# Performance work log

Measured on AMD Instinct MI355X. Metric: run time of the kernel, lower is better.

The kernel has to match this reference:

```python
import jax, jax.numpy as jnp
import numpy as np

B, H, W = 8, 128, 128
WIDTH, MODES = 32, 12
NL = 6


def _spectral_conv(x, w):
    # x: [B,C,H,W] real; w: [2, Cin, Cout, m, m, 2] (real/imag packed)
    b, c, h, ww = x.shape
    m = w.shape[3]
    xf = jnp.fft.rfft2(x)  # [B,C,H,W//2+1] complex
    w1 = w[0, ..., 0] + 1j * w[0, ..., 1]
    w2 = w[1, ..., 0] + 1j * w[1, ..., 1]
    top = jnp.einsum('bixy,ioxy->boxy', xf[:, :, :m, :m], w1)
    bot = jnp.einsum('bixy,ioxy->boxy', xf[:, :, -m:, :m], w2)
    out = jnp.zeros((b, w.shape[2], h, ww // 2 + 1), dtype=xf.dtype)
    out = out.at[:, :, :m, :m].set(top).at[:, :, -m:, :m].set(bot)
    return jnp.fft.irfft2(out, s=(h, ww))


def _conv1x1(x, wgt, bia):
    # x: [B,C,H,W], wgt: [O,C], bia: [O]
    return jnp.einsum('bchw,oc->bohw', x, wgt) + bia[None, :, None, None]


def _gelu(x):
    return jax.nn.gelu(x, approximate=False)


def setup_inputs() -> dict:
    key = jax.random.key(0)
    ks = jax.random.split(key, 20)
    scale = 1.0 / (WIDTH * WIDTH)
    d = {}
    d['x'] = jax.random.normal(ks[0], (B, H, W, 4), jnp.float32)
    d['fc0_W'] = jax.random.normal(ks[1], (4, WIDTH), jnp.float32) * 0.5
    d['fc0_b'] = jnp.zeros((WIDTH,), jnp.float32)
    d['spec_w'] = scale * jax.random.uniform(ks[2], (NL, 2, WIDTH, WIDTH, MODES, MODES, 2), jnp.float32)
    d['wW'] = jax.random.normal(ks[3], (NL, WIDTH, WIDTH), jnp.float32) * (1.0 / np.sqrt(WIDTH))
    d['wb'] = jnp.zeros((NL, WIDTH), jnp.float32)
    d['bW'] = jax.random.normal(ks[4], (NL, WIDTH, 2), jnp.float32) * 0.7
    d['bb'] = jnp.zeros((NL, WIDTH), jnp.float32)
    d['cW'] = jax.random.normal(ks[5], (NL, WIDTH, 3), jnp.float32) * 0.57
    d['cb'] = jnp.zeros((NL, WIDTH), jnp.float32)
    d['fc1_W'] = jax.random.normal(ks[6], (WIDTH, 256), jnp.float32) * (1.0 / np.sqrt(WIDTH))
    d['fc1_b'] = jnp.zeros((256,), jnp.float32)
    d['fc3_W'] = jax.random.normal(ks[7], (256, 128), jnp.float32) * (1.0 / 16.0)
    d['fc3_b'] = jnp.zeros((128,), jnp.float32)
    d['fc4_W'] = jax.random.normal(ks[8], (128, 128), jnp.float32) * (1.0 / np.sqrt(128.0))
    d['fc4_b'] = jnp.zeros((128,), jnp.float32)
    d['fc5_W'] = jax.random.normal(ks[9], (128, 1), jnp.float32) * (1.0 / np.sqrt(128.0))
    d['fc5_b'] = jnp.zeros((1,), jnp.float32)
    return d


def reference(x, fc0_W, fc0_b, spec_w, wW, wb, bW, bb, cW, cb,
              fc1_W, fc1_b, fc3_W, fc3_b, fc4_W, fc4_b, fc5_W, fc5_b):
    b, h, w, _ = x.shape
    grid_mesh = jnp.transpose(x[:, :, :, 1:4], (0, 3, 1, 2))  # [B,3,H,W]
    y = x @ fc0_W + fc0_b                                     # [B,H,W,width]
    y = jnp.transpose(y, (0, 3, 1, 2))                        # [B,width,H,W]
    gx = jnp.linspace(0.0, 1.0, h, dtype=jnp.float32)
    gy = jnp.linspace(0.0, 1.0, w, dtype=jnp.float32)
    grid = jnp.stack([
        jnp.broadcast_to(gx[:, None], (h, w)),
        jnp.broadcast_to(gy[None, :], (h, w)),
    ], axis=0)                                                # [2,H,W]
    grid = jnp.broadcast_to(grid[None], (b, 2, h, w))
    for l in range(NL):
        y = _gelu(_spectral_conv(y, spec_w[l])
                  + _conv1x1(y, wW[l], wb[l])
                  + _conv1x1(grid, bW[l], bb[l])
                  + _conv1x1(grid_mesh, cW[l], cb[l]))
    y = jnp.transpose(y, (0, 2, 3, 1))                        # [B,H,W,width]
    y = _gelu(y @ fc1_W + fc1_b)
    y = _gelu(y @ fc3_W + fc3_b)
    y = y @ fc4_W + fc4_b
    y = y @ fc5_W + fc5_b
    return y
```

## Files before the change

kernel.cpp:

```cpp
#include <hip/hip_runtime.h>
#include <math.h>


#define NL 6

typedef unsigned short u16;
typedef __attribute__((ext_vector_type(8))) short short8v;
typedef __attribute__((ext_vector_type(8))) unsigned short ushort8v;
typedef __attribute__((ext_vector_type(4))) unsigned short ushort4v;
typedef __attribute__((ext_vector_type(4))) float f32x4;

__device__ __forceinline__ float gelu_f(float x){
  float z  = x*0.70710678118654752f;
  float az = fabsf(z);
  float t  = __builtin_amdgcn_rcpf(fmaf(0.3275911f, az, 1.0f));
  float p  = t*(0.254829592f + t*(-0.284496736f + t*(1.421413741f +
             t*(-1.453152027f + t*1.061405429f))));
  float e  = __expf(-z*z);
  float er = copysignf(fmaf(-p, e, 1.0f), z);
  return 0.5f*x*(1.0f + er);
}
__device__ __forceinline__ u16 f2bf(float x){
  unsigned u = __float_as_uint(x);
  u += 0x7FFF + ((u>>16)&1);
  return (u16)(u>>16);
}
__device__ __forceinline__ float bf2f(u16 h){
  return __uint_as_float(((unsigned)h)<<16);
}
__device__ __forceinline__ void split2(float v, u16 &hh, u16 &ll){
  unsigned u = __float_as_uint(v);
  hh = (u16)(u>>16);
  float lo = v - __uint_as_float(u & 0xFFFF0000u);
  ll = (u16)(__float_as_uint(lo)>>16);
}

__global__ __launch_bounds__(256) void k_fc0f(const float* __restrict__ x,
                      const float* __restrict__ W, const float* __restrict__ b,
                      float* __restrict__ y, float* __restrict__ F1){
  __shared__ float Ws[128];
  __shared__ float bs[32];
  __shared__ float ys2[2][32][132];
  int t = threadIdx.x;
  if (t < 128) Ws[t] = W[t];
  if (t < 32)  bs[t] = b[t];
  __syncthreads();
  int pix = blockIdx.x*256 + t;
  float4 xv = *reinterpret_cast<const float4*>(x + (size_t)pix*4);
  int bb = pix >> 14, hw = pix & 16383;
  int r = t>>7, w = t&127;
  float* yp = y + (size_t)bb*32*16384 + hw;
  #pragma unroll
  for (int c=0;c<32;c++){
    float acc = bs[c] + xv.x*Ws[c] + xv.y*Ws[32+c] + xv.z*Ws[64+c] + xv.w*Ws[96+c];
    yp[(size_t)c*16384] = acc;
    ys2[r][c][w] = acc;
  }
  __syncthreads();
  int c2 = t>>3, wq = t&7;
  float stc[12], sts[12];
  #pragma unroll
  for (int k=0;k<12;k++){ float s,c; sincospif(k*(1.0f/64.0f), &s, &c); stc[k]=c; sts[k]=s; }
  int gr0 = blockIdx.x*2;
  #pragma unroll
  for (int r2=0;r2<2;r2++){
    float cr[12], ci[12], aR[12], aI[12];
    #pragma unroll
    for (int k=0;k<12;k++){
      float s,c; sincospif((float)(k*wq)*0.25f, &s, &c);
      cr[k]=c; ci[k]=s; aR[k]=0.f; aI[k]=0.f;
    }
    const float* rowp = &ys2[r2][c2][wq*16];
    #pragma unroll
    for (int q=0;q<4;q++){
      float4 xq = *reinterpret_cast<const float4*>(rowp + q*4);
      float xa[4]={xq.x,xq.y,xq.z,xq.w};
      #pragma unroll
      for (int e=0;e<4;e++){
        float xw = xa[e];
        #pragma unroll
        for (int k=0;k<12;k++){
          aR[k] += xw*cr[k];
          aI[k] -= xw*ci[k];
          float nc = cr[k]*stc[k] - ci[k]*sts[k];
          ci[k]    = cr[k]*sts[k] + ci[k]*stc[k];
          cr[k] = nc;
        }
      }
    }
    #pragma unroll
    for (int k=0;k<12;k++){
      aR[k] += __shfl_xor(aR[k],1); aR[k] += __shfl_xor(aR[k],2); aR[k] += __shfl_xor(aR[k],4);
      aI[k] += __shfl_xor(aI[k],1); aI[k] += __shfl_xor(aI[k],2); aI[k] += __shfl_xor(aI[k],4);
    }
    if (wq==0){
      int g = gr0 + r2; int b2 = g>>7, h2 = g&127;
      float* dst = F1 + ((size_t)(b2*32+c2)*128 + h2)*24;
      #pragma unroll
      for (int k=0;k<12;k++){ dst[2*k] = aR[k]; dst[2*k+1] = aI[k]; }
    }
  }
}

__global__ __launch_bounds__(256) void k_wtrans(const float* __restrict__ w, float* __restrict__ wT){
  __shared__ float buf[16][32][25];
  int t=threadIdx.x;
  int beta = blockIdx.x;
  int l = beta/48, r = beta%48;
  int hf = r/24; int r2 = r%24;
  int kym = r2>>1; int i0 = (r2&1)*16;
  const float* src = w + (size_t)l*589824 + (size_t)hf*294912 + kym*24;
  float* dst = wT + (size_t)l*589824 + (size_t)hf*294912 + (size_t)kym*24576;
  for (int j=t; j<12288; j+=256){
    int i = j/768, rem = j%768, o = rem/24, kxri = rem%24;
    buf[i][o][kxri] = src[(size_t)(i0+i)*9216 + o*288 + kxri];
  }
  __syncthreads();
  for (int j=t; j<12288; j+=256){
    int kx = j>>10, rem = j&1023, i = rem>>6, orr = rem&63, o = orr>>1, ri = orr&1;
    dst[(size_t)kx*2048 + o*64 + (i0+i)*2 + ri] = buf[i][o][kx*2+ri];
  }
}

__global__ __launch_bounds__(256) void k_wprep(const float* __restrict__ W1, const float* __restrict__ W3,
                       const float* __restrict__ W4,
                       const float* __restrict__ b4, const float* __restrict__ w5,
                       const float* __restrict__ b5,
                       u16* __restrict__ W1h, u16* __restrict__ W1l,
                       u16* __restrict__ W3h, u16* __restrict__ W3l,
                       u16* __restrict__ W4h, u16* __restrict__ W4l,
                       u16* __restrict__ Emh, u16* __restrict__ Eml,
                       float* __restrict__ c45){
  __shared__ float buf[32][132];
  int t = threadIdx.x, bid = blockIdx.x;
  if (bid < 8){
    int k0 = bid*32;
    for (int i=t;i<4096;i+=256){ int k=i>>7, n=i&127; buf[k][n] = W3[(size_t)(k0+k)*128 + n]; }
    __syncthreads();
    int n = t>>1, kq = t&1;
    #pragma unroll
    for (int kk=0;kk<16;kk++){
      int k = kq*16 + kk;
      float v = buf[k][n];
      u16 hh = f2bf(v);
      W3h[(size_t)bid*4096 + n*32 + k] = hh;
      W3l[(size_t)bid*4096 + n*32 + k] = f2bf(v - bf2f(hh));
    }
  } else if (bid == 8){
    __shared__ float red[256];
    int n = t;
    #pragma unroll
    for (int c=0;c<32;c++){
      float v = W1[(size_t)c*256 + n];
      u16 hh = f2bf(v);
      W1h[n*32 + c] = hh;
      W1l[n*32 + c] = f2bf(v - bf2f(hh));
    }
    red[t] = (t<128)? b4[t]*w5[t] : 0.f;
    __syncthreads();
    for (int s2=128; s2>0; s2>>=1){
      if (t<s2) red[t] += red[t+s2];
      __syncthreads();
    }
    if (t==0) c45[0] = red[0] + b5[0];
  } else if (bid <= 12){
    int k0 = (bid-9)*32;
    for (int i=t;i<4096;i+=256){ int k=i>>7, n=i&127; buf[k][n] = W4[(size_t)(k0+k)*128 + n]; }
    __syncthreads();
    int n = t>>1, kq = t&1;
    #pragma unroll
    for (int kk=0;kk<16;kk++){
      int k = kq*16 + kk;
      float v = buf[k][n];
      u16 hh = f2bf(v);
      W4h[(size_t)(bid-9)*4096 + n*32 + k] = hh;
      W4l[(size_t)(bid-9)*4096 + n*32 + k] = f2bf(v - bf2f(hh));
    }
  } else {
    for (int i=t;i<4096;i+=256){
      int m=i>>7, w=i&127;
      float v=0.f;
      if (m<24){ float s,c; sincospif((float)((m>>1)*w)*(1.0f/64.0f), &s, &c); v = (m&1)? -s : c; }
      u16 hh, ll; split2(v, hh, ll);
      Emh[i]=hh; Eml[i]=ll;
    }
  }
}

__global__ __launch_bounds__(576) void k_dfth(const float* __restrict__ F1, float* __restrict__ F2){
  __shared__ float fs[3072];
  int t=threadIdx.x;
  int bc = blockIdx.x;
  int b = bc>>5, c = bc&31;
  const float* src = F1 + (size_t)bc*3072;
  for (int i=t;i<3072;i+=576) fs[i] = src[i];
  __syncthreads();
  int pair = t>>1, half = t&1;
  int kx = pair%12, kyi = pair/12;
  int ky = (kyi<12)? kyi : kyi+104;
  float cs, ss; sincospif((float)ky*(1.0f/64.0f), &ss, &cs);
  float aR=0.f, aI=0.f;
  #pragma unroll
  for (int hq=0; hq<2; hq++){
    int h0 = half*64 + hq*32;
    int m0 = (ky*h0)&127;
    float c0,s0; sincospif((float)m0*(1.0f/64.0f), &s0, &c0);
    #pragma unroll 8
    for (int hh=0; hh<32; hh++){
      int h = h0+hh;
      float2 a = *reinterpret_cast<const float2*>(&fs[h*24 + 2*kx]);
      aR += a.x*c0 + a.y*s0;
      aI += a.y*c0 - a.x*s0;
      float nc = c0*cs - s0*ss; s0 = c0*ss + s0*cs; c0 = nc;
    }
  }
  aR += __shfl_xor(aR,1);
  aI += __shfl_xor(aI,1);
  if (half==0){
    float* dst = F2 + (((size_t)b*24 + kyi)*24 + 2*kx)*32 + c;
    dst[0]  = aR;
    dst[32] = aI;
  }
}

__global__ __launch_bounds__(576) void k_mixid(const float* __restrict__ F2, const float* __restrict__ wTl,
                      float* __restrict__ S1){
  __shared__ float Gs[24][28];
  int t=threadIdx.x;
  int bo = blockIdx.x;
  int b = bo>>5, o = bo&31;
  {
    int pair = t>>1, half = t&1;
    int kx = pair%12, kyi = pair/12;
    int hf = kyi<12?0:1, kym = kyi<12?kyi:kyi-12;
    const float* fpr = F2 + (((size_t)b*24 + kyi)*24 + 2*kx)*32 + half*16;
    const float* fpi = fpr + 32;
    const float* wp = wTl + (size_t)(hf*12+kym)*24576 + kx*2048 + o*64 + half*32;
    float gr=0.f, gi=0.f;
    #pragma unroll 8
    for (int i=0;i<16;i++){
      float2 wv = *reinterpret_cast<const float2*>(wp + 2*i);
      float ar = fpr[i], ai = fpi[i];
      gr += ar*wv.x - ai*wv.y;
      gi += ar*wv.y + ai*wv.x;
    }
    gr += __shfl_xor(gr,1);
    gi += __shfl_xor(gi,1);
    if (half==0){ Gs[kyi][2*kx] = gr; Gs[kyi][2*kx+1] = gi; }
  }
  __syncthreads();
  if (t < 512){
    int h = t>>2, q = t&3;
    float aR[12], aI[12];
    #pragma unroll
    for (int k=0;k<12;k++){ aR[k]=0.f; aI[k]=0.f; }
    float sc,ss; sincospif(h*(1.0f/64.0f), &ss, &sc);
    int ky0 = (q<2)? q*6 : 116 + (q-2)*6;
    float c0,s0;
    { int m0 = (ky0*h)&127; sincospif((float)m0*(1.0f/64.0f), &s0, &c0); }
    #pragma unroll
    for (int j=0;j<6;j++){
      int kyi = q*6 + j;
      float a[24];
      #pragma unroll
      for (int q2=0;q2<6;q2++) *reinterpret_cast<float4*>(&a[4*q2]) = *reinterpret_cast<const float4*>(&Gs[kyi][4*q2]);
      #pragma unroll
      for (int k=0;k<12;k++){
        aR[k] += a[2*k]*c0 - a[2*k+1]*s0;
        aI[k] += a[2*k]*s0 + a[2*k+1]*c0;
      }
      float nc = c0*sc - s0*ss; s0 = c0*ss + s0*sc; c0 = nc;
    }
    #pragma unroll
    for (int k=0;k<12;k++){
      aR[k] += __shfl_xor(aR[k], 1); aR[k] += __shfl_xor(aR[k], 2);
      aI[k] += __shfl_xor(aI[k], 1); aI[k] += __shfl_xor(aI[k], 2);
    }
    float* dst = S1 + ((size_t)bo*128 + h)*24;
    #pragma unroll
    for (int r=0;r<3;r++){
      int k = q*3 + r;
      dst[2*k]   = aR[k]*(1.0f/16384.0f);
      dst[2*k+1] = aI[k]*(1.0f/16384.0f);
    }
  }
}

template<int LAST>
__global__ __launch_bounds__(512) void k_combine2(const float* __restrict__ yin, const float* __restrict__ S1,
                         const float* __restrict__ x,
                         const float* __restrict__ wWl, const float* __restrict__ wbl,
                         const float* __restrict__ bWl, const float* __restrict__ bbl,
                         const float* __restrict__ cWl, const float* __restrict__ cbl,
                         const u16* __restrict__ Emh, const u16* __restrict__ Eml,
                         float* __restrict__ yout, float* __restrict__ F1,
                         u16* __restrict__ yh, u16* __restrict__ yl){
  __shared__ float ysT[128][33];
  __shared__ u16 ybsp[2][32][136];
  int t=threadIdx.x;
  int b = blockIdx.x>>7, h = blockIdx.x&127;
  for (int i=t;i<4096;i+=512){ int c=i>>7, w=i&127;
    ysT[w][c] = yin[(((size_t)(b*32+c))*128+h)*128+w]; }
  __syncthreads();
  int w = t&127;
  int og = __builtin_amdgcn_readfirstlane(t>>7);
  float ct[12], st[12];
  ct[0]=1.f; st[0]=0.f;
  float c1,s1v; sincospif(w*(1.0f/64.0f), &s1v, &c1);
  #pragma unroll
  for (int k=0;k<11;k++){ ct[k+1] = ct[k]*c1 - st[k]*s1v; st[k+1] = ct[k]*s1v + st[k]*c1; }
  float gx = h*(1.0f/127.0f), gy = w*(1.0f/127.0f);
  float4 xm = *reinterpret_cast<const float4*>(x + (((size_t)(b*128+h))*128+w)*4);
  float m1=xm.y, m2=xm.z, m3=xm.w;
  const float* wo  = wWl + og*256;
  const float* s1o = S1 + (size_t)b*98304 + (size_t)og*8*3072 + h*24;
  float accv[8];
  #pragma unroll
  for (int oi=0;oi<8;oi++){
    int o = og*8+oi;
    float bse = wbl[o] + bbl[o] + cbl[o] + gx*bWl[o*2] + gy*bWl[o*2+1]
              + m1*cWl[o*3] + m2*cWl[o*3+1] + m3*cWl[o*3+2];
    const float* sp = s1o + (size_t)oi*3072;
    float spec = sp[0];
    #pragma unroll
    for (int kx=1;kx<12;kx++) spec += 2.0f*(sp[2*kx]*ct[kx] - sp[2*kx+1]*st[kx]);
    accv[oi] = bse + spec;
  }
  #pragma unroll
  for (int c=0;c<32;c++){
    float xc = ysT[w][c];
    #pragma unroll
    for (int oi=0;oi<8;oi++) accv[oi] += wo[oi*32+c]*xc;
  }
  #pragma unroll
  for (int oi=0;oi<8;oi++){
    float g = gelu_f(accv[oi]);
    u16 hh, ll; split2(g, hh, ll);
    int o = og*8+oi;
    ybsp[0][o][w] = hh;
    ybsp[1][o][w] = ll;
    if constexpr (!LAST)
      yout[(((size_t)(b*32+o))*128+h)*128+w] = g;
  }
  __syncthreads();
  if constexpr (!LAST){
    int wv = t>>6;
    if (wv < 4){
      int lane = t&63, lr = lane&15, lg = lane>>4;
      int mt = wv&1, oj = wv>>1;
      f32x4 acc = (f32x4){0.f,0.f,0.f,0.f};
      #pragma unroll
      for (int ks=0; ks<4; ++ks){
        short8v ef = *reinterpret_cast<const short8v*>(Emh + (size_t)(mt*16+lr)*128 + ks*32 + lg*8);
        short8v eg = *reinterpret_cast<const short8v*>(Eml + (size_t)(mt*16+lr)*128 + ks*32 + lg*8);
        short8v yf = *reinterpret_cast<const short8v*>(&ybsp[0][oj*16+lr][ks*32+lg*8]);
        short8v yg = *reinterpret_cast<const short8v*>(&ybsp[1][oj*16+lr][ks*32+lg*8]);
        acc = __builtin_amdgcn_mfma_f32_16x16x32_bf16(ef, yf, acc, 0,0,0);
        acc = __builtin_amdgcn_mfma_f32_16x16x32_bf16(ef, yg, acc, 0,0,0);
        acc = __builtin_amdgcn_mfma_f32_16x16x32_bf16(eg, yf, acc, 0,0,0);
      }
      if (mt==0 || lg<2){
        int m = mt*16 + 4*lg;
        int o = oj*16 + lr;
        float4 v; v.x=acc[0]; v.y=acc[1]; v.z=acc[2]; v.w=acc[3];
        *reinterpret_cast<float4*>(&F1[((size_t)(b*32+o)*128 + h)*24 + m]) = v;
      }
    }
  } else {
    int wr = t>>2, hf4 = t&3;
    size_t pix = (size_t)b*16384 + h*128 + wr;
    ushort8v h8, l8;
    #pragma unroll
    for (int q=0;q<8;q++){
      h8[q] = ybsp[0][hf4*8 + q][wr];
      l8[q] = ybsp[1][hf4*8 + q][wr];
    }
    *reinterpret_cast<ushort8v*>(yh + pix*32 + hf4*8) = h8;
    *reinterpret_cast<ushort8v*>(yl + pix*32 + hf4*8) = l8;
  }
}

__global__ __launch_bounds__(256) void k_headm(
    const u16* __restrict__ Yh, const u16* __restrict__ Yl,
    const u16* __restrict__ W1h, const u16* __restrict__ W1l,
    const float* __restrict__ b1,
    const u16* __restrict__ W3h, const u16* __restrict__ W3l,
    const float* __restrict__ b3,
    const u16* __restrict__ W4h, const u16* __restrict__ W4l,
    const float* __restrict__ c45, const float* __restrict__ w5,
    float* __restrict__ out){
  __shared__ u16 smem[17408];
  __shared__ float b1s[256];
  __shared__ float b3s[128], w5s[128];
  __shared__ float part2[2][64];
  int t = threadIdx.x;
  int wv = t>>6, lane = t&63, lr = lane&15, lg = lane>>4;
  int P0 = blockIdx.x*64;
  b1s[t] = b1[t];
  if (t<128){ b3s[t]=b3[t]; w5s[t]=w5[t]; }
  int wn3 = wv>>1, wp = wv&1;
  short8v ybh, ybl;
  {
    size_t p = (size_t)P0 + wv*16 + lr;
    ybh = *reinterpret_cast<const short8v*>(Yh + p*32 + lg*8);
    ybl = *reinterpret_cast<const short8v*>(Yl + p*32 + lg*8);
  }
  f32x4 acc3[4][2];
  #pragma unroll
  for (int i=0;i<4;i++){ acc3[i][0]=(f32x4){0,0,0,0}; acc3[i][1]=(f32x4){0,0,0,0}; }
  __syncthreads();

  auto fc1_into = [&](int kt, u16* dh, u16* dl){
    f32x4 a1[2];
    a1[0]=(f32x4){0,0,0,0}; a1[1]=(f32x4){0,0,0,0};
    #pragma unroll
    for (int i=0;i<2;i++){
      int n1 = kt*32 + i*16 + lr;
      short8v w1f = *reinterpret_cast<const short8v*>(W1h + (size_t)n1*32 + lg*8);
      short8v w1g = *reinterpret_cast<const short8v*>(W1l + (size_t)n1*32 + lg*8);
      a1[i] = __builtin_amdgcn_mfma_f32_16x16x32_bf16(w1f, ybh, a1[i], 0,0,0);
      a1[i] = __builtin_amdgcn_mfma_f32_16x16x32_bf16(w1f, ybl, a1[i], 0,0,0);
      a1[i] = __builtin_amdgcn_mfma_f32_16x16x32_bf16(w1g, ybh, a1[i], 0,0,0);
    }
    #pragma unroll
    for (int i=0;i<2;i++){
      int n1b = kt*32 + i*16 + 4*lg;
      int p = wv*16 + lr;
      ushort4v hv, lv;
      #pragma unroll
      for (int r=0;r<4;r++){
        float v = gelu_f(a1[i][r] + b1s[n1b+r]);
        u16 hh, ll; split2(v, hh, ll);
        hv[r] = hh; lv[r] = ll;
      }
      *reinterpret_cast<ushort4v*>(&dh[p*40 + i*16+4*lg]) = hv;
      *reinterpret_cast<ushort4v*>(&dl[p*40 + i*16+4*lg]) = lv;
    }
  };

  fc1_into(0, smem, smem + 2560);
  __syncthreads();
  for (int kt=0; kt<8; ++kt){
    u16* curh = (kt&1)? smem + 5120 : smem;
    u16* curl = curh + 2560;
    if (kt < 7){
      u16* nh = (kt&1)? smem : smem + 5120;
      fc1_into(kt+1, nh, nh + 2560);
    }
    short8v abh[2], abl[2];
    #pragma unroll
    for (int j=0;j<2;j++){
      int pb = wp*32 + j*16 + lr;
      abh[j] = *reinterpret_cast<const short8v*>(&curh[pb*40 + lg*8]);
      abl[j] = *reinterpret_cast<const short8v*>(&curl[pb*40 + lg*8]);
    }
    #pragma unroll
    for (int i=0;i<4;i++){
      int n3 = wn3*64 + i*16 + lr;
      short8v w3f = *reinterpret_cast<const short8v*>(W3h + (size_t)kt*4096 + n3*32 + lg*8);
      short8v w3g = *reinterpret_cast<const short8v*>(W3l + (size_t)kt*4096 + n3*32 + lg*8);
      #pragma unroll
      for (int j=0;j<2;j++){
        acc3[i][j] = __builtin_amdgcn_mfma_f32_16x16x32_bf16(w3f, abh[j], acc3[i][j], 0,0,0);
        acc3[i][j] = __builtin_amdgcn_mfma_f32_16x16x32_bf16(w3f, abl[j], acc3[i][j], 0,0,0);
        acc3[i][j] = __builtin_amdgcn_mfma_f32_16x16x32_bf16(w3g, abh[j], acc3[i][j], 0,0,0);
      }
    }
    __syncthreads();
  }
  u16* A2h = smem;
  u16* A2l = smem + 8704;
  #pragma unroll
  for (int i=0;i<4;i++){
    int n3b = wn3*64 + i*16 + 4*lg;
    #pragma unroll
    for (int j=0;j<2;j++){
      int p = wp*32 + j*16 + lr;
      ushort4v hv, lv;
      #pragma unroll
      for (int r=0;r<4;r++){
        float v = gelu_f(acc3[i][j][r] + b3s[n3b+r]);
        u16 hh, ll; split2(v, hh, ll);
        hv[r] = hh; lv[r] = ll;
      }
      *reinterpret_cast<ushort4v*>(&A2h[p*136 + n3b]) = hv;
      *reinterpret_cast<ushort4v*>(&A2l[p*136 + n3b]) = lv;
    }
  }
  __syncthreads();
  f32x4 acc4[4][2];
  #pragma unroll
  for (int i=0;i<4;i++){ acc4[i][0]=(f32x4){0,0,0,0}; acc4[i][1]=(f32x4){0,0,0,0}; }
  #pragma unroll
  for (int ks=0; ks<4; ++ks){
    short8v p2h[2], p2l[2];
    #pragma unroll
    for (int j=0;j<2;j++){
      int p = wp*32 + j*16 + lr;
      p2h[j] = *reinterpret_cast<const short8v*>(&A2h[p*136 + ks*32 + lg*8]);
      p2l[j] = *reinterpret_cast<const short8v*>(&A2l[p*136 + ks*32 + lg*8]);
    }
    #pragma unroll
    for (int i2=0;i2<4;i2++){
      int n4 = wn3*64 + i2*16 + lr;
      short8v w4f = *reinterpret_cast<const short8v*>(W4h + (size_t)ks*4096 + n4*32 + lg*8);
      short8v w4g = *reinterpret_cast<const short8v*>(W4l + (size_t)ks*4096 + n4*32 + lg*8);
      #pragma unroll
      for (int j=0;j<2;j++){
        acc4[i2][j] = __builtin_amdgcn_mfma_f32_16x16x32_bf16(w4f, p2h[j], acc4[i2][j], 0,0,0);
        acc4[i2][j] = __builtin_amdgcn_mfma_f32_16x16x32_bf16(w4f, p2l[j], acc4[i2][j], 0,0,0);
        acc4[i2][j] = __builtin_amdgcn_mfma_f32_16x16x32_bf16(w4g, p2h[j], acc4[i2][j], 0,0,0);
      }
    }
  }
  #pragma unroll
  for (int j=0;j<2;j++){
    float part = 0.f;
    #pragma unroll
    for (int i2=0;i2<4;i2++){
      #pragma unroll
      for (int r=0;r<4;r++){
        int n4 = wn3*64 + i2*16 + 4*lg + r;
        part += acc4[i2][j][r] * w5s[n4];
      }
    }
    part += __shfl_xor(part, 16); part += __shfl_xor(part, 32);
    if (lg==0) part2[wn3][wp*32 + j*16 + lr] = part;
  }
  __syncthreads();
  if (t<64) out[P0 + t] = part2[0][t] + part2[1][t] + c45[0];
}

extern "C" void kernel_launch(void* const* d_in, const int* in_sizes, int n_in,
                              void* d_out, int out_size, void* d_ws, size_t ws_size,
                              hipStream_t stream){
  const float* x     = (const float*)d_in[0];
  const float* fc0_W = (const float*)d_in[1];
  const float* fc0_b = (const float*)d_in[2];
  const float* spec_w= (const float*)d_in[3];
  const float* wW    = (const float*)d_in[4];
  const float* wb    = (const float*)d_in[5];
  const float* bW    = (const float*)d_in[6];
  const float* bb    = (const float*)d_in[7];
  const float* cW    = (const float*)d_in[8];
  const float* cb    = (const float*)d_in[9];
  const float* fc1_W = (const float*)d_in[10];
  const float* fc1_b = (const float*)d_in[11];
  const float* fc3_W = (const float*)d_in[12];
  const float* fc3_b = (const float*)d_in[13];
  const float* fc4_W = (const float*)d_in[14];
  const float* fc4_b = (const float*)d_in[15];
  const float* fc5_W = (const float*)d_in[16];
  const float* fc5_b = (const float*)d_in[17];
  float* out = (float*)d_out;
  float* ws  = (float*)d_ws;

  float* y_a = ws;
  float* y_b = y_a + 4194304;
  float* wT  = y_b + 4194304;
  float* F2  = wT + 3538944;
  float* S1  = F2 + 147456;
  float* F1  = S1 + 786432;
  float* WP  = F1 + 786432;
  u16*   W1h = (u16*)WP;
  u16*   W1l = W1h + 8192;
  u16*   W3h = W1l + 8192;
  u16*   W3l = W3h + 32768;
  u16*   W4h = W3l + 32768;
  u16*   W4l = W4h + 16384;
  u16*   Emh = W4l + 16384;
  u16*   Eml = Emh + 4096;
  float* c45 = (float*)(Eml + 4096);
  u16*   Yhh  = (u16*)y_a;
  u16*   Yll_ = (u16*)y_a + 4194304;

  k_fc0f<<<512,256,0,stream>>>(x, fc0_W, fc0_b, y_a, F1);
  k_wtrans<<<288,256,0,stream>>>(spec_w, wT);
  k_wprep<<<14,256,0,stream>>>(fc1_W, fc3_W, fc4_W, fc4_b, fc5_W, fc5_b,
                               W1h, W1l, W3h, W3l, W4h, W4l, Emh, Eml, c45);

  for (int l=0;l<NL;l++){
    float* yin  = (l&1)? y_b : y_a;
    float* yout = (l&1)? y_a : y_b;
    k_dfth<<<256,576,0,stream>>>(F1, F2);
    k_mixid<<<256,576,0,stream>>>(F2, wT + (size_t)l*589824, S1);
    if (l < NL-1){
      k_combine2<0><<<1024,512,0,stream>>>(yin, S1, x,
                                     wW + (size_t)l*1024, wb + (size_t)l*32,
                                     bW + (size_t)l*64,  bb + (size_t)l*32,
                                     cW + (size_t)l*96,  cb + (size_t)l*32,
                                     Emh, Eml,
                                     yout, F1, nullptr, nullptr);
    } else {
      k_combine2<1><<<1024,512,0,stream>>>(yin, S1, x,
                                     wW + (size_t)l*1024, wb + (size_t)l*32,
                                     bW + (size_t)l*64,  bb + (size_t)l*32,
                                     cW + (size_t)l*96,  cb + (size_t)l*32,
                                     Emh, Eml,
                                     nullptr, nullptr, Yhh, Yll_);
    }
  }

  k_headm<<<2048,256,0,stream>>>(Yhh, Yll_, W1h, W1l, fc1_b, W3h, W3l, fc3_b,
                                 W4h, W4l, c45, fc5_W, out);
}
```

Baseline: 344.1 us.

## Replace scalar DFT loops in dfth and mixid with split-bf16 MFMA GEMMs

The H-direction forward DFT in k_dfth and the inverse H-direction DFT in k_mixid are rewritten as small matrix multiplies on MFMA units. They use precomputed twiddle matrices (E2, E3), built in two new k_wprep blocks, and bf16 hi/lo splitting to keep roughly fp32 accuracy. This removes per-thread sincos recurrences and scalar FMA chains. In exchange it adds extra MFMA passes for the split precision, some padding zeroing in shared memory, and a smaller block size for dfth.

```diff
diff --git a/kernel.cpp b/kernel.cpp
--- a/kernel.cpp
+++ b/kernel.cpp
@@ -130,6 +130,8 @@
                        u16* __restrict__ W3h, u16* __restrict__ W3l,
                        u16* __restrict__ W4h, u16* __restrict__ W4l,
                        u16* __restrict__ Emh, u16* __restrict__ Eml,
+                       u16* __restrict__ E2h, u16* __restrict__ E2l,
+                       u16* __restrict__ E3h, u16* __restrict__ E3l,
                        float* __restrict__ c45){
   __shared__ float buf[32][132];
   int t = threadIdx.x, bid = blockIdx.x;
@@ -176,7 +178,7 @@
       W4h[(size_t)(bid-9)*4096 + n*32 + k] = hh;
       W4l[(size_t)(bid-9)*4096 + n*32 + k] = f2bf(v - bf2f(hh));
     }
-  } else {
+  } else if (bid == 13){
     for (int i=t;i<4096;i+=256){
       int m=i>>7, w=i&127;
       float v=0.f;
@@ -184,51 +186,90 @@
       u16 hh, ll; split2(v, hh, ll);
       Emh[i]=hh; Eml[i]=ll;
     }
-  }
-}
-
-__global__ __launch_bounds__(576) void k_dfth(const float* __restrict__ F1, float* __restrict__ F2){
-  __shared__ float fs[3072];
+  } else if (bid == 14){
+    for (int i=t;i<12288;i+=256){
+      int m=i>>8, k=i&255;
+      int kyi = (m<24)? m : m-24;
+      int ky  = (kyi<12)? kyi : kyi+104;
+      int h   = k&127;
+      int mm  = (ky*h)&127;
+      float s,c; sincospif((float)mm*(1.0f/64.0f), &s, &c);
+      bool sinSlot = k>=128;
+      float v;
+      if (m<24) v = sinSlot? s : c;
+      else      v = sinSlot? c : -s;
+      u16 hh, ll; split2(v, hh, ll);
+      E2h[i]=hh; E2l[i]=ll;
+    }
+  } else {
+    for (int i=t;i<8192;i+=256){
+      int h=i>>6, k=i&63;
+      float v=0.f;
+      if (k<48){
+        int kyi = (k<24)? k : k-24;
+        int ky  = (kyi<12)? kyi : kyi+104;
+        int mm  = (ky*h)&127;
+        float s,c; sincospif((float)mm*(1.0f/64.0f), &s, &c);
+        v = ((k<24)? c : s) * (1.0f/16384.0f);
+      }
+      u16 hh, ll; split2(v, hh, ll);
+      E3h[i]=hh; E3l[i]=ll;
+    }
+  }
+}
+
+__global__ __launch_bounds__(256) void k_dfth(const float* __restrict__ F1,
+                      const u16* __restrict__ E2h, const u16* __restrict__ E2l,
+                      float* __restrict__ F2){
+  __shared__ u16 Fth[16*264], Ftl[16*264];
   int t=threadIdx.x;
   int bc = blockIdx.x;
   int b = bc>>5, c = bc&31;
   const float* src = F1 + (size_t)bc*3072;
-  for (int i=t;i<3072;i+=576) fs[i] = src[i];
-  __syncthreads();
-  int pair = t>>1, half = t&1;
-  int kx = pair%12, kyi = pair/12;
-  int ky = (kyi<12)? kyi : kyi+104;
-  float cs, ss; sincospif((float)ky*(1.0f/64.0f), &ss, &cs);
-  float aR=0.f, aI=0.f;
-  #pragma unroll
-  for (int hq=0; hq<2; hq++){
-    int h0 = half*64 + hq*32;
-    int m0 = (ky*h0)&127;
-    float c0,s0; sincospif((float)m0*(1.0f/64.0f), &s0, &c0);
-    #pragma unroll 8
-    for (int hh=0; hh<32; hh++){
-      int h = h0+hh;
-      float2 a = *reinterpret_cast<const float2*>(&fs[h*24 + 2*kx]);
-      aR += a.x*c0 + a.y*s0;
-      aI += a.y*c0 - a.x*s0;
-      float nc = c0*cs - s0*ss; s0 = c0*ss + s0*cs; c0 = nc;
-    }
-  }
-  aR += __shfl_xor(aR,1);
-  aI += __shfl_xor(aI,1);
-  if (half==0){
-    float* dst = F2 + (((size_t)b*24 + kyi)*24 + 2*kx)*32 + c;
-    dst[0]  = aR;
-    dst[32] = aI;
+  for (int i=t;i<3072;i+=256){
+    int h = i/24, col = i - h*24;
+    int kx = col>>1, ri = col&1;
+    u16 hh, ll; split2(src[i], hh, ll);
+    int idx = kx*264 + ri*128 + h;
+    Fth[idx] = hh; Ftl[idx] = ll;
+  }
+  __syncthreads();
+  int wv = t>>6, lane = t&63, lr = lane&15, lg = lane>>4;
+  if (wv < 3){
+    f32x4 acc = (f32x4){0.f,0.f,0.f,0.f};
+    #pragma unroll
+    for (int ks=0; ks<8; ++ks){
+      short8v af = *reinterpret_cast<const short8v*>(E2h + (size_t)(wv*16+lr)*256 + ks*32 + lg*8);
+      short8v ag = *reinterpret_cast<const short8v*>(E2l + (size_t)(wv*16+lr)*256 + ks*32 + lg*8);
+      short8v bf = *reinterpret_cast<const short8v*>(&Fth[lr*264 + ks*32 + lg*8]);
+      short8v bg = *reinterpret_cast<const short8v*>(&Ftl[lr*264 + ks*32 + lg*8]);
+      acc = __builtin_amdgcn_mfma_f32_16x16x32_bf16(af, bf, acc, 0,0,0);
+      acc = __builtin_amdgcn_mfma_f32_16x16x32_bf16(af, bg, acc, 0,0,0);
+      acc = __builtin_amdgcn_mfma_f32_16x16x32_bf16(ag, bf, acc, 0,0,0);
+    }
+    if (lr < 12){
+      #pragma unroll
+      for (int r=0;r<4;r++){
+        int m = wv*16 + 4*lg + r;
+        int kyi = (m<24)? m : m-24;
+        int ri  = (m<24)? 0 : 1;
+        F2[(((size_t)b*24 + kyi)*24 + 2*lr + ri)*32 + c] = acc[r];
+      }
+    }
   }
 }
 
 __global__ __launch_bounds__(576) void k_mixid(const float* __restrict__ F2, const float* __restrict__ wTl,
+                      const u16* __restrict__ E3h, const u16* __restrict__ E3l,
                       float* __restrict__ S1){
-  __shared__ float Gs[24][28];
+  __shared__ u16 Bh[32*72], Bl[32*72];
   int t=threadIdx.x;
   int bo = blockIdx.x;
   int b = bo>>5, o = bo&31;
+  for (int i=t; i<24*24; i+=576){
+    int row = i/24, k = 48 + i - (i/24)*24;
+    Bh[row*72 + k] = 0; Bl[row*72 + k] = 0;
+  }
   {
     int pair = t>>1, half = t&1;
     int kx = pair%12, kyi = pair/12;
@@ -246,42 +287,48 @@
     }
     gr += __shfl_xor(gr,1);
     gi += __shfl_xor(gi,1);
-    if (half==0){ Gs[kyi][2*kx] = gr; Gs[kyi][2*kx+1] = gi; }
-  }
-  __syncthreads();
-  if (t < 512){
-    int h = t>>2, q = t&3;
-    float aR[12], aI[12];
-    #pragma unroll
-    for (int k=0;k<12;k++){ aR[k]=0.f; aI[k]=0.f; }
-    float sc,ss; sincospif(h*(1.0f/64.0f), &ss, &sc);
-    int ky0 = (q<2)? q*6 : 116 + (q-2)*6;
-    float c0,s0;
-    { int m0 = (ky0*h)&127; sincospif((float)m0*(1.0f/64.0f), &s0, &c0); }
-    #pragma unroll
-    for (int j=0;j<6;j++){
-      int kyi = q*6 + j;
-      float a[24];
-      #pragma unroll
-      for (int q2=0;q2<6;q2++) *reinterpret_cast<float4*>(&a[4*q2]) = *reinterpret_cast<const float4*>(&Gs[kyi][4*q2]);
-      #pragma unroll
-      for (int k=0;k<12;k++){
-        aR[k] += a[2*k]*c0 - a[2*k+1]*s0;
-        aI[k] += a[2*k]*s0 + a[2*k+1]*c0;
-      }
-      float nc = c0*sc - s0*ss; s0 = c0*ss + s0*sc; c0 = nc;
-    }
-    #pragma unroll
-    for (int k=0;k<12;k++){
-      aR[k] += __shfl_xor(aR[k], 1); aR[k] += __shfl_xor(aR[k], 2);
-      aI[k] += __shfl_xor(aI[k], 1); aI[k] += __shfl_xor(aI[k], 2);
-    }
-    float* dst = S1 + ((size_t)bo*128 + h)*24;
-    #pragma unroll
-    for (int r=0;r<3;r++){
-      int k = q*3 + r;
-      dst[2*k]   = aR[k]*(1.0f/16384.0f);
-      dst[2*k+1] = aI[k]*(1.0f/16384.0f);
+    if (half==0){
+      u16 grh, grl, gih, gil, nih, nil;
+      split2(gr, grh, grl);
+      split2(gi, gih, gil);
+      split2(-gi, nih, nil);
+      int r0 = (2*kx)*72, r1 = (2*kx+1)*72;
+      Bh[r0 + kyi]      = grh; Bl[r0 + kyi]      = grl;
+      Bh[r0 + 24 + kyi] = nih; Bl[r0 + 24 + kyi] = nil;
+      Bh[r1 + kyi]      = gih; Bl[r1 + kyi]      = gil;
+      Bh[r1 + 24 + kyi] = grh; Bl[r1 + 24 + kyi] = grl;
+    }
+  }
+  __syncthreads();
+  int wv = t>>6, lane = t&63, lr = lane&15, lg = lane>>4;
+  if (wv < 8){
+    f32x4 acc[2];
+    acc[0] = (f32x4){0.f,0.f,0.f,0.f};
+    acc[1] = (f32x4){0.f,0.f,0.f,0.f};
+    #pragma unroll
+    for (int ks=0; ks<2; ++ks){
+      short8v af = *reinterpret_cast<const short8v*>(E3h + (size_t)(wv*16+lr)*64 + ks*32 + lg*8);
+      short8v ag = *reinterpret_cast<const short8v*>(E3l + (size_t)(wv*16+lr)*64 + ks*32 + lg*8);
+      #pragma unroll
+      for (int nt=0; nt<2; ++nt){
+        short8v bf = *reinterpret_cast<const short8v*>(&Bh[(nt*16+lr)*72 + ks*32 + lg*8]);
+        short8v bg = *reinterpret_cast<const short8v*>(&Bl[(nt*16+lr)*72 + ks*32 + lg*8]);
+        acc[nt] = __builtin_amdgcn_mfma_f32_16x16x32_bf16(af, bf, acc[nt], 0,0,0);
+        acc[nt] = __builtin_amdgcn_mfma_f32_16x16x32_bf16(af, bg, acc[nt], 0,0,0);
+        acc[nt] = __builtin_amdgcn_mfma_f32_16x16x32_bf16(ag, bf, acc[nt], 0,0,0);
+      }
+    }
+    float* dst = S1 + (size_t)bo*3072;
+    #pragma unroll
+    for (int nt=0; nt<2; ++nt){
+      int n = nt*16 + lr;
+      if (n < 24){
+        #pragma unroll
+        for (int r=0;r<4;r++){
+          int h = wv*16 + 4*lg + r;
+          dst[h*24 + n] = acc[nt][r];
+        }
+      }
     }
   }
 }
@@ -570,20 +617,25 @@
   u16*   W4l = W4h + 16384;
   u16*   Emh = W4l + 16384;
   u16*   Eml = Emh + 4096;
-  float* c45 = (float*)(Eml + 4096);
+  u16*   E2h = Eml + 4096;
+  u16*   E2l = E2h + 12288;
+  u16*   E3h = E2l + 12288;
+  u16*   E3l = E3h + 8192;
+  float* c45 = (float*)(E3l + 8192);
   u16*   Yhh  = (u16*)y_a;
   u16*   Yll_ = (u16*)y_a + 4194304;
 
   k_fc0f<<<512,256,0,stream>>>(x, fc0_W, fc0_b, y_a, F1);
   k_wtrans<<<288,256,0,stream>>>(spec_w, wT);
-  k_wprep<<<14,256,0,stream>>>(fc1_W, fc3_W, fc4_W, fc4_b, fc5_W, fc5_b,
-                               W1h, W1l, W3h, W3l, W4h, W4l, Emh, Eml, c45);
+  k_wprep<<<16,256,0,stream>>>(fc1_W, fc3_W, fc4_W, fc4_b, fc5_W, fc5_b,
+                               W1h, W1l, W3h, W3l, W4h, W4l, Emh, Eml,
+                               E2h, E2l, E3h, E3l, c45);
 
   for (int l=0;l<NL;l++){
     float* yin  = (l&1)? y_b : y_a;
     float* yout = (l&1)? y_a : y_b;
-    k_dfth<<<256,576,0,stream>>>(F1, F2);
-    k_mixid<<<256,576,0,stream>>>(F2, wT + (size_t)l*589824, S1);
+    k_dfth<<<256,256,0,stream>>>(F1, E2h, E2l, F2);
+    k_mixid<<<256,576,0,stream>>>(F2, wT + (size_t)l*589824, E3h, E3l, S1);
     if (l < NL-1){
       k_combine2<0><<<1024,512,0,stream>>>(yin, S1, x,
                                      wW + (size_t)l*1024, wb + (size_t)l*32,
```

After: 336.8 us. 1.02x faster.
